# Optimization experiments

Hardware: AMD Instinct MI355X
Metric: run time of the kernel (lower is better)

The kernel has to match this reference:

```python
import jax, jax.numpy as jnp
import numpy as np

FEATURES = 4096
BATCH = 2048


def setup_inputs() -> dict:
    key = jax.random.key(0)
    kx, kk = jax.random.split(key)
    x = jax.random.normal(kx, (BATCH, FEATURES), dtype=jnp.float32)
    kernel = jax.random.normal(kk, (FEATURES,), dtype=jnp.float32)
    return {"x": x, "kernel": kernel}


def reference(x, kernel):
    n = kernel.shape[0]
    i = jnp.arange(n)[:, None]   # [n,1]
    j = jnp.arange(n)[None, :]   # [1,n]
    idx = i - j                   # Toeplitz offsets
    # W[i,j] = kernel[i-j] if i>=j else 0  (causal lower-triangular Toeplitz)
    W = jnp.where(idx >= 0, kernel[jnp.clip(idx, 0, n - 1)], 0.0)
    # out[b,i] = sum_{j<=i} x[b,j] * kernel[i-j]  == x @ W.T
    return x @ W.T
```

## Files before the change

kernel.cpp:

```cpp
#include <hip/hip_runtime.h>
#include <hip/hip_bf16.h>


typedef unsigned short u16;
typedef __attribute__((ext_vector_type(8))) short  bf16x8;
typedef __attribute__((ext_vector_type(8))) unsigned short u16x8;
typedef __attribute__((ext_vector_type(4))) float  f32x4;

#define KDIM 4096
#define NDIM 4096
#define MDIM 2048
#define KREV_STRIDE 4608
#define KREV_BYTES  (8 * KREV_STRIDE * 2)

#define MFMA_BF16 __builtin_amdgcn_mfma_f32_16x16x32_bf16

static __device__ inline u16 f2bf(float f) {
  unsigned u = __builtin_bit_cast(unsigned, f);
  unsigned r = u + 0x7FFFu + ((u >> 16) & 1u);
  return (u16)(r >> 16);
}

static __device__ inline void async_copy16(const void* g, void* l) {
  __builtin_amdgcn_global_load_lds((const __attribute__((address_space(1))) void*)g,
                                   (__attribute__((address_space(3))) void*)l,
                                   16, 0, 0);
}

__global__ __launch_bounds__(256) void prep(const float* __restrict__ x,
                                            const float* __restrict__ kern,
                                            u16* __restrict__ xb,
                                            u16* __restrict__ krevs,
                                            int conv_blocks) {
  int kblk = (int)blockIdx.x - conv_blocks;
  if (kblk >= 0) {
    int u = kblk * 256 + threadIdx.x;
    for (int a = 0; a < 8; ++a) {
      int t = u + a - 8;
      u16 v = 0;
      if (t >= 0 && t <= 4095) v = f2bf(kern[4095 - t]);
      krevs[a * KREV_STRIDE + u] = v;
    }
  } else {
    unsigned tg  = blockIdx.x * 256 + threadIdx.x;
    unsigned l   = tg & 63;
    unsigned kb  = (tg >> 6) & 127;
    unsigned rg  = tg >> 13;
    unsigned row = rg * 16 + (l & 15);
    unsigned k   = kb * 32 + (l >> 4) * 8;
    const f32x4* p = (const f32x4*)(x + (size_t)row * KDIM + k);
    f32x4 v0 = p[0], v1 = p[1];
    u16x8 r;
    r[0] = f2bf(v0[0]); r[1] = f2bf(v0[1]); r[2] = f2bf(v0[2]); r[3] = f2bf(v0[3]);
    r[4] = f2bf(v1[0]); r[5] = f2bf(v1[1]); r[6] = f2bf(v1[2]); r[7] = f2bf(v1[3]);
    *(u16x8*)(xb + (size_t)tg * 8) = r;
  }
}

template <bool CONV>
__global__ __launch_bounds__(512, 4) void toeplitz_gemm(const void* __restrict__ Av,
                                                        const u16* __restrict__ krevs,
                                                        float* __restrict__ out) {
  __shared__ __align__(16) char smem_raw[73984];
  u16*   B_all = (u16*)smem_raw;
  f32x4* ep    = (f32x4*)smem_raw;

  const int tid  = threadIdx.x;
  const int w    = tid >> 6;
  const int g    = w >> 2;
  const int wl   = w & 3;
  const int lane = tid & 63;
  const int lane16 = lane & 15;
  const int quad   = lane >> 4;
  const int wm = wl >> 1;
  const int wn = wl & 1;

  const int b   = (int)blockIdx.x;
  const int x_  = b & 7;
  const int jj  = b >> 3;
  const int p_  = x_ + 8 * (jj & 1);
  const int mt2 = p_ * 2 + ((jj >> 1) & 1);
  const int ctp = jj >> 2;
  const int ct1 = 31 - ctp;
  const int ct2 = ctp;
  const int m0  = mt2 * 64;

  const int len1 = 128 * (ct1 + 1) + 160, stride1 = len1 + 40;
  const int len2 = 128 * (ct2 + 1) + 160, stride2 = len2 + 40;
  const int base2 = 8 * stride1;
  const int W1 = 3968 - 128 * ct1;
  const int W2 = 3968 - 128 * ct2;

  const int wmu = __builtin_amdgcn_readfirstlane(wm);
  const int gu  = __builtin_amdgcn_readfirstlane(g);
  const u16*   xb2 = (const u16*)Av;
  const float* xf  = (const float*)Av;
  int aoffs[2];
  for (int fm = 0; fm < 2; ++fm)
    aoffs[fm] = (mt2 * 4 + wmu * 2 + fm) * 65536 + gu * 1024 + lane * 8;
  const int rowb = m0 + wm * 32 + lane16;

  auto ldA = [&](int fm, int t, int kk) -> bf16x8 {
    return *(const bf16x8*)(xb2 + aoffs[fm] + t * 2048 + kk * 512);
  };
  auto ldAc = [&](int fm, int t, int kk) -> bf16x8 {
    const float* px = xf + (size_t)(rowb + fm * 16) * KDIM +
                      t * 128 + gu * 64 + kk * 32 + quad * 8;
    f32x4 v0 = *(const f32x4*)px, v1 = *(const f32x4*)(px + 4);
    u16x8 r;
    r[0]=f2bf(v0[0]); r[1]=f2bf(v0[1]); r[2]=f2bf(v0[2]); r[3]=f2bf(v0[3]);
    r[4]=f2bf(v1[0]); r[5]=f2bf(v1[1]); r[6]=f2bf(v1[2]); r[7]=f2bf(v1[3]);
    return __builtin_bit_cast(bf16x8, r);
  };

  auto stageWin = [&](int base_e, int stride_e, int len_e, int Wp) {
    const u16* src = krevs + w * KREV_STRIDE + Wp;
    char* dstb = smem_raw + (size_t)(base_e + w * stride_e) * 2;
    for (int c = 0; c * 512 < len_e; ++c) {
      int idx = c * 512 + lane * 8;
      if (idx < len_e)
        async_copy16(src + idx, dstb + (size_t)c * 1024);
    }
  };
  stageWin(0, stride1, len1, W1);
  stageWin(base2, stride2, len2, W2);
  asm volatile("s_waitcnt vmcnt(0)" ::: "memory");
  __builtin_amdgcn_s_barrier();
  asm volatile("" ::: "memory");

  auto runPhase = [&](int ctq, int base_e, int stride_q, int Wq) {
    const int n0q = ctq * 128;
    int boff[4];
    for (int fn = 0; fn < 4; ++fn) {
      int n_g = n0q + wn * 64 + fn * 16 + lane16;
      int s0  = 4095 - n_g + quad * 8;
      int a   = s0 & 7;
      boff[fn] = base_e + a * stride_q + (s0 - a + 8 - Wq);
    }
    f32x4 acc[2][4] = {};

    if constexpr (!CONV) {
      bf16x8 afA[2], afB[2], bvA[4], bvB[4];
#pragma unroll
      for (int fm = 0; fm < 2; ++fm) afA[fm] = ldA(fm, 0, 0);
#pragma unroll
      for (int fm = 0; fm < 2; ++fm) afB[fm] = ldA(fm, 0, 1);
#pragma unroll
      for (int fn = 0; fn < 4; ++fn)
        bvA[fn] = *(const bf16x8*)(&B_all[boff[fn] + g * 64]);
      for (int t = 0; ; ++t) {
        const int ks = t * 128 + g * 64;
#pragma unroll
        for (int fn = 0; fn < 4; ++fn)
          bvB[fn] = *(const bf16x8*)(&B_all[boff[fn] + ks + 32]);
#pragma unroll
        for (int fn = 0; fn < 4; ++fn)
#pragma unroll
          for (int fm = 0; fm < 2; ++fm)
            acc[fm][fn] = MFMA_BF16(afA[fm], bvA[fn], acc[fm][fn], 0, 0, 0);
        if (t < ctq)
#pragma unroll
          for (int fm = 0; fm < 2; ++fm) afA[fm] = ldA(fm, t + 1, 0);
        if (t < ctq)
#pragma unroll
          for (int fn = 0; fn < 4; ++fn)
            bvA[fn] = *(const bf16x8*)(&B_all[boff[fn] + ks + 128]);
#pragma unroll
        for (int fn = 0; fn < 4; ++fn)
#pragma unroll
          for (int fm = 0; fm < 2; ++fm)
            acc[fm][fn] = MFMA_BF16(afB[fm], bvB[fn], acc[fm][fn], 0, 0, 0);
        if (t == ctq) break;
#pragma unroll
        for (int fm = 0; fm < 2; ++fm) afB[fm] = ldA(fm, t + 1, 1);
      }
    } else {
      for (int t = 0; t <= ctq; ++t) {
        const int ks = t * 128 + g * 64;
#pragma unroll
        for (int kk = 0; kk < 2; ++kk) {
          bf16x8 af[2];
#pragma unroll
          for (int fm = 0; fm < 2; ++fm) af[fm] = ldAc(fm, t, kk);
#pragma unroll
          for (int fn = 0; fn < 4; ++fn) {
            bf16x8 bv = *(const bf16x8*)(&B_all[boff[fn] + ks + kk * 32]);
#pragma unroll
            for (int fm = 0; fm < 2; ++fm)
              acc[fm][fn] = MFMA_BF16(af[fm], bv, acc[fm][fn], 0, 0, 0);
          }
        }
      }
    }

    const int j = tid & 255;
    __syncthreads();
    if (g == 1) {
      for (int fm = 0; fm < 2; ++fm)
        for (int fn = 0; fn < 4; ++fn)
          ep[j * 9 + fm * 4 + fn] = acc[fm][fn];
    }
    __syncthreads();
    if (g == 0) {
      for (int fm = 0; fm < 2; ++fm)
        for (int fn = 0; fn < 4; ++fn) {
          f32x4 v = acc[fm][fn];
          f32x4 o = ep[j * 9 + fm * 4 + fn];
          v[0] += o[0]; v[1] += o[1]; v[2] += o[2]; v[3] += o[3];
          int row_base = m0 + wm * 32 + fm * 16 + quad * 4;
          int col = n0q + wn * 64 + fn * 16 + lane16;
          for (int r = 0; r < 4; ++r)
            out[(size_t)(row_base + r) * NDIM + col] = v[r];
        }
    }
  };

  runPhase(ct1, 0, stride1, W1);
  runPhase(ct2, base2, stride2, W2);
}

extern "C" void kernel_launch(void* const* d_in, const int* in_sizes, int n_in,
                              void* d_out, int out_size, void* d_ws, size_t ws_size,
                              hipStream_t stream) {
  const float* x    = (const float*)d_in[0];
  const float* kern = (const float*)d_in[1];
  float* out = (float*)d_out;

  u16* krevs = (u16*)d_ws;
  u16* xb    = (u16*)((char*)d_ws + KREV_BYTES);
  const size_t need_fast = (size_t)KREV_BYTES + (size_t)MDIM * KDIM * 2;

  if (ws_size >= need_fast) {
    prep<<<4096 + 18, 256, 0, stream>>>(x, kern, xb, krevs, 4096);
    toeplitz_gemm<false><<<512, 512, 0, stream>>>(xb, krevs, out);
  } else {
    prep<<<18, 256, 0, stream>>>(x, kern, xb, krevs, 0);
    toeplitz_gemm<true><<<512, 512, 0, stream>>>(x, krevs, out);
  }
}
```

Before: 112.5 us.

## Repartition waves into 4-way split-K with 64x64 per-wave tiles

The eight waves change from a 2-way K split with 2x2 wave tiling (32x64 per wave) to a 4-way K split where each wave covers the full 64 rows and 64 columns. This doubles MFMA work per B-fragment LDS read and drops one A global load per step, so fewer loads feed more math. The cost is 64 accumulator registers per wave and a two-stage LDS tree reduction across the four K groups with extra barriers. The staged LDS window length is also simplified to cover the padded stride.

After: 151.1 us. 1.34x slower.

```diff
diff --git a/kernel.cpp b/kernel.cpp
--- a/kernel.cpp
+++ b/kernel.cpp
@@ -63,17 +63,16 @@
                                                         float* __restrict__ out) {
   __shared__ __align__(16) char smem_raw[73984];
   u16*   B_all = (u16*)smem_raw;
-  f32x4* ep    = (f32x4*)smem_raw;
+  f32x4* epA   = (f32x4*)smem_raw;
+  f32x4* epB   = (f32x4*)(smem_raw + 18432);
 
   const int tid  = threadIdx.x;
   const int w    = tid >> 6;
-  const int g    = w >> 2;
-  const int wl   = w & 3;
+  const int g    = w >> 1;
+  const int wn   = w & 1;
   const int lane = tid & 63;
   const int lane16 = lane & 15;
   const int quad   = lane >> 4;
-  const int wm = wl >> 1;
-  const int wn = wl & 1;
 
   const int b   = (int)blockIdx.x;
   const int x_  = b & 7;
@@ -85,27 +84,26 @@
   const int ct2 = ctp;
   const int m0  = mt2 * 64;
 
-  const int len1 = 128 * (ct1 + 1) + 160, stride1 = len1 + 40;
-  const int len2 = 128 * (ct2 + 1) + 160, stride2 = len2 + 40;
-  const int base2 = 8 * stride1;
+  const int stride1 = 128 * (ct1 + 1) + 200;
+  const int stride2 = 128 * (ct2 + 1) + 200;
+  const int base2   = 8 * stride1;
   const int W1 = 3968 - 128 * ct1;
   const int W2 = 3968 - 128 * ct2;
 
-  const int wmu = __builtin_amdgcn_readfirstlane(wm);
-  const int gu  = __builtin_amdgcn_readfirstlane(g);
+  const int gu = __builtin_amdgcn_readfirstlane(g);
   const u16*   xb2 = (const u16*)Av;
   const float* xf  = (const float*)Av;
-  int aoffs[2];
-  for (int fm = 0; fm < 2; ++fm)
-    aoffs[fm] = (mt2 * 4 + wmu * 2 + fm) * 65536 + gu * 1024 + lane * 8;
-  const int rowb = m0 + wm * 32 + lane16;
-
-  auto ldA = [&](int fm, int t, int kk) -> bf16x8 {
-    return *(const bf16x8*)(xb2 + aoffs[fm] + t * 2048 + kk * 512);
-  };
-  auto ldAc = [&](int fm, int t, int kk) -> bf16x8 {
+  int aoffs[4];
+  for (int fm = 0; fm < 4; ++fm)
+    aoffs[fm] = (mt2 * 4 + fm) * 65536 + gu * 512 + lane * 8;
+  const int rowb = m0 + lane16;
+
+  auto ldA = [&](int fm, int t) -> bf16x8 {
+    return *(const bf16x8*)(xb2 + aoffs[fm] + t * 2048);
+  };
+  auto ldAc = [&](int fm, int t) -> bf16x8 {
     const float* px = xf + (size_t)(rowb + fm * 16) * KDIM +
-                      t * 128 + gu * 64 + kk * 32 + quad * 8;
+                      t * 128 + gu * 32 + quad * 8;
     f32x4 v0 = *(const f32x4*)px, v1 = *(const f32x4*)(px + 4);
     u16x8 r;
     r[0]=f2bf(v0[0]); r[1]=f2bf(v0[1]); r[2]=f2bf(v0[2]); r[3]=f2bf(v0[3]);
@@ -113,17 +111,17 @@
     return __builtin_bit_cast(bf16x8, r);
   };
 
-  auto stageWin = [&](int base_e, int stride_e, int len_e, int Wp) {
+  auto stageWin = [&](int base_e, int stride_e, int Wp) {
     const u16* src = krevs + w * KREV_STRIDE + Wp;
     char* dstb = smem_raw + (size_t)(base_e + w * stride_e) * 2;
-    for (int c = 0; c * 512 < len_e; ++c) {
+    for (int c = 0; c * 512 < stride_e; ++c) {
       int idx = c * 512 + lane * 8;
-      if (idx < len_e)
+      if (idx < stride_e)
         async_copy16(src + idx, dstb + (size_t)c * 1024);
     }
   };
-  stageWin(0, stride1, len1, W1);
-  stageWin(base2, stride2, len2, W2);
+  stageWin(0, stride1, W1);
+  stageWin(base2, stride2, W2);
   asm volatile("s_waitcnt vmcnt(0)" ::: "memory");
   __builtin_amdgcn_s_barrier();
   asm volatile("" ::: "memory");
@@ -137,81 +135,110 @@
       int a   = s0 & 7;
       boff[fn] = base_e + a * stride_q + (s0 - a + 8 - Wq);
     }
-    f32x4 acc[2][4] = {};
+    f32x4 acc[4][4] = {};
 
     if constexpr (!CONV) {
-      bf16x8 afA[2], afB[2], bvA[4], bvB[4];
-#pragma unroll
-      for (int fm = 0; fm < 2; ++fm) afA[fm] = ldA(fm, 0, 0);
-#pragma unroll
-      for (int fm = 0; fm < 2; ++fm) afB[fm] = ldA(fm, 0, 1);
-#pragma unroll
-      for (int fn = 0; fn < 4; ++fn)
-        bvA[fn] = *(const bf16x8*)(&B_all[boff[fn] + g * 64]);
-      for (int t = 0; ; ++t) {
-        const int ks = t * 128 + g * 64;
-#pragma unroll
-        for (int fn = 0; fn < 4; ++fn)
-          bvB[fn] = *(const bf16x8*)(&B_all[boff[fn] + ks + 32]);
-#pragma unroll
-        for (int fn = 0; fn < 4; ++fn)
-#pragma unroll
-          for (int fm = 0; fm < 2; ++fm)
-            acc[fm][fn] = MFMA_BF16(afA[fm], bvA[fn], acc[fm][fn], 0, 0, 0);
-        if (t < ctq)
-#pragma unroll
-          for (int fm = 0; fm < 2; ++fm) afA[fm] = ldA(fm, t + 1, 0);
-        if (t < ctq)
-#pragma unroll
-          for (int fn = 0; fn < 4; ++fn)
-            bvA[fn] = *(const bf16x8*)(&B_all[boff[fn] + ks + 128]);
-#pragma unroll
-        for (int fn = 0; fn < 4; ++fn)
-#pragma unroll
-          for (int fm = 0; fm < 2; ++fm)
-            acc[fm][fn] = MFMA_BF16(afB[fm], bvB[fn], acc[fm][fn], 0, 0, 0);
-        if (t == ctq) break;
-#pragma unroll
-        for (int fm = 0; fm < 2; ++fm) afB[fm] = ldA(fm, t + 1, 1);
+      bf16x8 afA[4], afB[4];
+#pragma unroll
+      for (int fm = 0; fm < 4; ++fm) afA[fm] = ldA(fm, 0);
+      for (int t = 0; ; ) {
+        {
+          const int ks = t * 128 + g * 32;
+          bf16x8 bv[4];
+#pragma unroll
+          for (int fn = 0; fn < 4; ++fn)
+            bv[fn] = *(const bf16x8*)(&B_all[boff[fn] + ks]);
+          if (t < ctq)
+#pragma unroll
+            for (int fm = 0; fm < 4; ++fm) afB[fm] = ldA(fm, t + 1);
+#pragma unroll
+          for (int fn = 0; fn < 4; ++fn)
+#pragma unroll
+            for (int fm = 0; fm < 4; ++fm)
+              acc[fm][fn] = MFMA_BF16(afA[fm], bv[fn], acc[fm][fn], 0, 0, 0);
+          if (t == ctq) break;
+          ++t;
+        }
+        {
+          const int ks = t * 128 + g * 32;
+          bf16x8 bv[4];
+#pragma unroll
+          for (int fn = 0; fn < 4; ++fn)
+            bv[fn] = *(const bf16x8*)(&B_all[boff[fn] + ks]);
+          if (t < ctq)
+#pragma unroll
+            for (int fm = 0; fm < 4; ++fm) afA[fm] = ldA(fm, t + 1);
+#pragma unroll
+          for (int fn = 0; fn < 4; ++fn)
+#pragma unroll
+            for (int fm = 0; fm < 4; ++fm)
+              acc[fm][fn] = MFMA_BF16(afB[fm], bv[fn], acc[fm][fn], 0, 0, 0);
+          if (t == ctq) break;
+          ++t;
+        }
       }
     } else {
       for (int t = 0; t <= ctq; ++t) {
-        const int ks = t * 128 + g * 64;
-#pragma unroll
-        for (int kk = 0; kk < 2; ++kk) {
-          bf16x8 af[2];
-#pragma unroll
-          for (int fm = 0; fm < 2; ++fm) af[fm] = ldAc(fm, t, kk);
-#pragma unroll
-          for (int fn = 0; fn < 4; ++fn) {
-            bf16x8 bv = *(const bf16x8*)(&B_all[boff[fn] + ks + kk * 32]);
-#pragma unroll
-            for (int fm = 0; fm < 2; ++fm)
-              acc[fm][fn] = MFMA_BF16(af[fm], bv, acc[fm][fn], 0, 0, 0);
-          }
+        const int ks = t * 128 + g * 32;
+        bf16x8 af[4];
+#pragma unroll
+        for (int fm = 0; fm < 4; ++fm) af[fm] = ldAc(fm, t);
+#pragma unroll
+        for (int fn = 0; fn < 4; ++fn) {
+          bf16x8 bv = *(const bf16x8*)(&B_all[boff[fn] + ks]);
+#pragma unroll
+          for (int fm = 0; fm < 4; ++fm)
+            acc[fm][fn] = MFMA_BF16(af[fm], bv, acc[fm][fn], 0, 0, 0);
         }
       }
     }
 
-    const int j = tid & 255;
+    const int j9 = (wn * 64 + lane) * 9;
     __syncthreads();
-    if (g == 1) {
-      for (int fm = 0; fm < 2; ++fm)
-        for (int fn = 0; fn < 4; ++fn)
-          ep[j * 9 + fm * 4 + fn] = acc[fm][fn];
-    }
-    __syncthreads();
+#pragma unroll
+    for (int hh = 0; hh < 2; ++hh) {
+      if (g == 1)
+        for (int f2 = 0; f2 < 2; ++f2)
+          for (int fn = 0; fn < 4; ++fn)
+            epA[j9 + f2 * 4 + fn] = acc[hh * 2 + f2][fn];
+      if (g == 3)
+        for (int f2 = 0; f2 < 2; ++f2)
+          for (int fn = 0; fn < 4; ++fn)
+            epB[j9 + f2 * 4 + fn] = acc[hh * 2 + f2][fn];
+      __syncthreads();
+      if (g == 0)
+        for (int f2 = 0; f2 < 2; ++f2)
+          for (int fn = 0; fn < 4; ++fn)
+            acc[hh * 2 + f2][fn] += epA[j9 + f2 * 4 + fn];
+      if (g == 2)
+        for (int f2 = 0; f2 < 2; ++f2)
+          for (int fn = 0; fn < 4; ++fn)
+            acc[hh * 2 + f2][fn] += epB[j9 + f2 * 4 + fn];
+      __syncthreads();
+    }
+#pragma unroll
+    for (int hh = 0; hh < 2; ++hh) {
+      if (g == 2)
+        for (int f2 = 0; f2 < 2; ++f2)
+          for (int fn = 0; fn < 4; ++fn)
+            epA[j9 + f2 * 4 + fn] = acc[hh * 2 + f2][fn];
+      __syncthreads();
+      if (g == 0)
+        for (int f2 = 0; f2 < 2; ++f2)
+          for (int fn = 0; fn < 4; ++fn)
+            acc[hh * 2 + f2][fn] += epA[j9 + f2 * 4 + fn];
+      __syncthreads();
+    }
+
     if (g == 0) {
-      for (int fm = 0; fm < 2; ++fm)
+      for (int fm = 0; fm < 4; ++fm) {
+        int row_base = m0 + fm * 16 + quad * 4;
         for (int fn = 0; fn < 4; ++fn) {
-          f32x4 v = acc[fm][fn];
-          f32x4 o = ep[j * 9 + fm * 4 + fn];
-          v[0] += o[0]; v[1] += o[1]; v[2] += o[2]; v[3] += o[3];
-          int row_base = m0 + wm * 32 + fm * 16 + quad * 4;
           int col = n0q + wn * 64 + fn * 16 + lane16;
           for (int r = 0; r < 4; ++r)
-            out[(size_t)(row_base + r) * NDIM + col] = v[r];
-        }
+            out[(size_t)(row_base + r) * NDIM + col] = acc[fm][fn][r];
+        }
+      }
     }
   };
 
```
